# Optimization experiments

Measured on AMD Instinct MI355X. Metric: run time of the kernel, lower is better.

## Reference

```python
import jax, jax.numpy as jnp
import numpy as np

N, F, H, E = 100000, 128, 128, 3200000
EPS = 1e-5


def setup_inputs() -> dict:
    key = jax.random.key(0)
    ks = jax.random.split(key, 16)
    g = lambda k, shape, fan_in: jax.random.normal(k, shape, jnp.float32) / np.sqrt(fan_in)
    inp = {
        'x': jax.random.normal(ks[0], (N, F), jnp.float32),
        'edge_index': jax.random.randint(ks[1], (2, E), 0, N, jnp.int64),
        # SAGEConv params: lin_l (aggregated-neighbor path, has bias), lin_r (root path, no bias)
        'W1l': g(ks[2], (F, H), F), 'b1': jnp.zeros((H,), jnp.float32), 'W1r': g(ks[3], (F, H), F),
        'W2l': g(ks[4], (H, H), H), 'b2': jnp.zeros((H,), jnp.float32), 'W2r': g(ks[5], (H, H), H),
        'W3l': g(ks[6], (H, H), H), 'b3': jnp.zeros((H,), jnp.float32), 'W3r': g(ks[7], (H, H), H),
        'W4l': g(ks[8], (H, 1), H), 'b4': jnp.zeros((1,), jnp.float32), 'W4r': g(ks[9], (H, 1), H),
        # BatchNorm affine params
        'g1': jnp.ones((H,), jnp.float32), 'be1': jnp.zeros((H,), jnp.float32),
        'g2': jnp.ones((H,), jnp.float32), 'be2': jnp.zeros((H,), jnp.float32),
        'g3': jnp.ones((H,), jnp.float32), 'be3': jnp.zeros((H,), jnp.float32),
        # shared residual linear
        'Wlin': g(ks[10], (H, H), H), 'blin': jnp.zeros((H,), jnp.float32),
    }
    return inp


def _sage(x, src, dst, Wl, b, Wr):
    # mean aggregation of source features at destination nodes
    n = x.shape[0]
    s = jax.ops.segment_sum(x[src], dst, num_segments=n)          # [N, d]
    cnt = jax.ops.segment_sum(jnp.ones_like(dst, x.dtype), dst, num_segments=n)
    agg = s / jnp.maximum(cnt, 1.0)[:, None]
    return agg @ Wl + b + x @ Wr


def _bn(x, gamma, beta):
    # training-mode batch norm over node dim (biased variance, as torch)
    mu = x.mean(0)
    var = jnp.mean((x - mu) ** 2, axis=0)
    return gamma * (x - mu) * jax.lax.rsqrt(var + EPS) + beta


def reference(x, edge_index, W1l, b1, W1r, W2l, b2, W2r, W3l, b3, W3r,
              W4l, b4, W4r, g1, be1, g2, be2, g3, be3, Wlin, blin):
    src, dst = edge_index[0], edge_index[1]
    # dropout is identity (eval-mode reference)
    x1 = jax.nn.elu(_bn(_sage(x, src, dst, W1l, b1, W1r), g1, be1))
    x2 = jax.nn.elu(_bn(_sage(x1, src, dst, W2l, b2, W2r), g2, be2))
    x2 = x2 + x1 @ Wlin + blin
    x3 = jax.nn.elu(_bn(_sage(x2, src, dst, W3l, b3, W3r), g3, be3))
    x3 = x3 + x2 @ Wlin + blin
    x4 = _sage(x3, src, dst, W4l, b4, W4r)  # [N, 1]
    return jnp.squeeze(x4, -1)
```

## Files before the change

### kernel.cpp

```cpp
#include <hip/hip_runtime.h>
#include <hip/hip_bf16.h>
#include <math.h>

#define BN_EPS 1e-5f

typedef __attribute__((ext_vector_type(8))) short bf16x8;
typedef __attribute__((ext_vector_type(4))) float f32x4;
typedef unsigned int uint32;

__device__ __forceinline__ unsigned bf16rne(float f) {
  unsigned u = __float_as_uint(f);
  unsigned r = u + 0x7fffu + ((u >> 16) & 1u);
  return r >> 16;
}
__device__ __forceinline__ float bf2f_lo(uint32 u) { return __uint_as_float(u << 16); }
__device__ __forceinline__ float bf2f_hi(uint32 u) { return __uint_as_float(u & 0xffff0000u); }
__device__ __forceinline__ uint32 packbf2(float a, float b) {
  return bf16rne(a) | (bf16rne(b) << 16);
}

__device__ __forceinline__ int edge_at(const int* __restrict__ ei, long long idx, int is64) {
  return is64 ? ei[2 * idx] : ei[idx];
}

__global__ void detect_kernel(const int* __restrict__ ei, long long E, int* __restrict__ flag) {
  __shared__ int found;
  int t = threadIdx.x;
  if (t == 0) found = 0;
  __syncthreads();
  long long npairs = E < 1024 ? E : 1024;
  for (long long p = t; p < npairs; p += blockDim.x)
    if (ei[2 * p + 1] != 0) found = 1;
  __syncthreads();
  if (t == 0) *flag = found ? 0 : 1;
}

__global__ void zero_i32_kernel(int* __restrict__ p, long long n) {
  long long i = blockIdx.x * (long long)blockDim.x + threadIdx.x;
  if (i < n) p[i] = 0;
}
__global__ void zero_f32_kernel(float* __restrict__ p, long long n) {
  long long i = blockIdx.x * (long long)blockDim.x + threadIdx.x;
  if (i < n) p[i] = 0.f;
}

__global__ void extract_count_kernel(const int* __restrict__ ei, long long E,
                                     const int* __restrict__ flag,
                                     int* __restrict__ es, int* __restrict__ r8,
                                     int* __restrict__ cnt8, int N) {
  long long e = blockIdx.x * (long long)blockDim.x + threadIdx.x;
  if (e >= E) return;
  int is64 = *flag;
  es[e] = edge_at(ei, e, is64);
  int d = edge_at(ei, E + e, is64);
  int sh = blockIdx.x & 7;
  r8[e] = atomicAdd(&cnt8[(size_t)sh * N + d], 1);
}

__global__ void cumnode_kernel(const int* __restrict__ cnt8, int* __restrict__ cum8,
                               int* __restrict__ cnt_node, int N) {
  int n = blockIdx.x * blockDim.x + threadIdx.x;
  if (n >= N) return;
  int run = 0;
#pragma unroll
  for (int sh = 0; sh < 8; ++sh) {
    int c = cnt8[(size_t)sh * N + n];
    cum8[(size_t)sh * N + n] = run;
    run += c;
  }
  cnt_node[n] = run;
}

__global__ void partial_kernel(const int* __restrict__ cnt, int* __restrict__ bsum, int M) {
  __shared__ int s[256];
  int b = blockIdx.x, t = threadIdx.x;
  int base = b * 2048 + t * 8;
  int sum = 0;
#pragma unroll
  for (int i = 0; i < 8; ++i) {
    int idx = base + i;
    if (idx < M) sum += cnt[idx];
  }
  s[t] = sum;
  __syncthreads();
  for (int d = 128; d > 0; d >>= 1) {
    if (t < d) s[t] += s[t + d];
    __syncthreads();
  }
  if (t == 0) bsum[b] = s[0];
}

__global__ void scanb_kernel(int* __restrict__ bsum, int nb) {
  __shared__ int s[512];
  int t = threadIdx.x;
  int v = (t < nb) ? bsum[t] : 0;
  s[t] = v;
  __syncthreads();
  for (int d = 1; d < 512; d <<= 1) {
    int u = (t >= d) ? s[t - d] : 0;
    __syncthreads();
    s[t] += u;
    __syncthreads();
  }
  if (t < nb) bsum[t] = s[t] - v;
}

__global__ void offsets_kernel(const int* __restrict__ cnt, const int* __restrict__ bsum,
                               int* __restrict__ off, int M, long long Etot) {
  __shared__ int s[256];
  int b = blockIdx.x, t = threadIdx.x;
  int base = b * 2048 + t * 8;
  int v[8];
  int sum = 0;
#pragma unroll
  for (int i = 0; i < 8; ++i) {
    int idx = base + i;
    v[i] = (idx < M) ? cnt[idx] : 0;
    sum += v[i];
  }
  s[t] = sum;
  __syncthreads();
  for (int d = 1; d < 256; d <<= 1) {
    int u = (t >= d) ? s[t - d] : 0;
    __syncthreads();
    s[t] += u;
    __syncthreads();
  }
  int run = bsum[b] + s[t] - sum;
#pragma unroll
  for (int i = 0; i < 8; ++i) {
    int idx = base + i;
    if (idx < M) {
      off[idx] = run;
      run += v[i];
    }
  }
  if (b == 0 && t == 0) off[M] = (int)Etot;
}

__global__ void pos_kernel(const int* __restrict__ ei, long long E, const int* __restrict__ flag,
                           const int* __restrict__ r8, const int* __restrict__ off_node,
                           const int* __restrict__ cum8, uint32* __restrict__ ppk, int N) {
  long long e = blockIdx.x * (long long)blockDim.x + threadIdx.x;
  if (e >= E) return;
  int is64 = *flag;
  int d = edge_at(ei, E + e, is64);
  int sh = blockIdx.x & 7;
  uint32 pos = (uint32)(off_node[d] + cum8[(size_t)sh * N + d] + r8[e]);
  uint32 region = (uint32)d >> 15;
  ppk[e] = pos | (region << 28);
}

__global__ void scatter_det_kernel(const int* __restrict__ es, const uint32* __restrict__ ppk,
                                   long long E, uint32 p, int* __restrict__ esrc) {
  long long e = blockIdx.x * (long long)blockDim.x + threadIdx.x;
  if (e >= E) return;
  uint32 v = ppk[e];
  if ((v >> 28) == p) esrc[v & 0x0FFFFFFFu] = es[e];
}

__global__ void convert_bf16_kernel(const float* __restrict__ x, uint32* __restrict__ xb,
                                    long long total2) {
  long long i = blockIdx.x * (long long)blockDim.x + threadIdx.x;
  if (i >= total2) return;
  float2 f = ((const float2*)x)[i];
  xb[i] = packbf2(f.x, f.y);
}

__global__ void repack_all_kernel(const float* __restrict__ Wa, const float* __restrict__ Wb,
                                  const float* __restrict__ Wc, const float* __restrict__ Wd,
                                  const float* __restrict__ We, const float* __restrict__ Wf,
                                  const float* __restrict__ Wg, ushort* __restrict__ Wp) {
  int wi = blockIdx.x >> 3;
  const float* W = wi == 0 ? Wa : wi == 1 ? Wb : wi == 2 ? Wc : wi == 3 ? Wd
                 : wi == 4 ? We : wi == 5 ? Wf : Wg;
  ushort* dst = Wp + (size_t)wi * 16384;
  int s = (blockIdx.x & 7) * 256 + threadIdx.x;
  int nt = s >> 8, rem = s & 255, ks = rem >> 6, lane = rem & 63;
  int q = lane >> 4, l16 = lane & 15;
  int kbase = ks * 32 + q * 8, c = nt * 16 + l16;
  uint32 out[4];
#pragma unroll
  for (int jp = 0; jp < 4; ++jp) {
    float a = W[(size_t)(kbase + 2 * jp) * 128 + c];
    float b = W[(size_t)(kbase + 2 * jp + 1) * 128 + c];
    out[jp] = packbf2(a, b);
  }
  ((uint4*)dst)[s] = make_uint4(out[0], out[1], out[2], out[3]);
}

__global__ void aggregate_bf16_kernel(const uint32* __restrict__ X, const int* __restrict__ off,
                                      const int* __restrict__ esrc, uint32* __restrict__ out,
                                      int N) {
  int gw = (int)((blockIdx.x * (long long)blockDim.x + threadIdx.x) >> 6);
  int lane = threadIdx.x & 63;
  if (gw >= N) return;
  int b = off[gw], e = off[gw + 1];
  int sub = lane & 15, grp = lane >> 4;
  const uint4* X4 = (const uint4*)X;
  float acc[8];
#pragma unroll
  for (int j = 0; j < 8; ++j) acc[j] = 0.f;
  for (int i = b; i < e; i += 8) {
    int i0 = i + grp, i1 = i + 4 + grp;
    bool h0 = i0 < e, h1 = i1 < e;
    uint4 v0 = make_uint4(0, 0, 0, 0), v1 = make_uint4(0, 0, 0, 0);
    if (h0) { int s0 = esrc[i0]; v0 = X4[(size_t)s0 * 16 + sub]; }
    if (h1) { int s1 = esrc[i1]; v1 = X4[(size_t)s1 * 16 + sub]; }
    if (h0) {
      acc[0] += bf2f_lo(v0.x); acc[1] += bf2f_hi(v0.x);
      acc[2] += bf2f_lo(v0.y); acc[3] += bf2f_hi(v0.y);
      acc[4] += bf2f_lo(v0.z); acc[5] += bf2f_hi(v0.z);
      acc[6] += bf2f_lo(v0.w); acc[7] += bf2f_hi(v0.w);
    }
    if (h1) {
      acc[0] += bf2f_lo(v1.x); acc[1] += bf2f_hi(v1.x);
      acc[2] += bf2f_lo(v1.y); acc[3] += bf2f_hi(v1.y);
      acc[4] += bf2f_lo(v1.z); acc[5] += bf2f_hi(v1.z);
      acc[6] += bf2f_lo(v1.w); acc[7] += bf2f_hi(v1.w);
    }
  }
#pragma unroll
  for (int j = 0; j < 8; ++j) {
    acc[j] += __shfl_xor(acc[j], 16, 64);
    acc[j] += __shfl_xor(acc[j], 32, 64);
  }
  if (grp == 0) {
    float inv = 1.0f / fmaxf((float)(e - b), 1.0f);
    uint4 o;
    o.x = packbf2(acc[0] * inv, acc[1] * inv);
    o.y = packbf2(acc[2] * inv, acc[3] * inv);
    o.z = packbf2(acc[4] * inv, acc[5] * inv);
    o.w = packbf2(acc[6] * inv, acc[7] * inv);
    ((uint4*)out)[(size_t)gw * 16 + sub] = o;
  }
}

__launch_bounds__(256)
__global__ void gemm_mfma_kernel(const ushort* __restrict__ A1, const ushort* __restrict__ W1p,
                                 const ushort* __restrict__ A2, const ushort* __restrict__ W2p,
                                 const ushort* __restrict__ W3p,
                                 const float* __restrict__ bias, const float* __restrict__ rbias,
                                 ushort* __restrict__ Y, ushort* __restrict__ R,
                                 float* __restrict__ bnsum, int N) {
  __shared__ float sred[16][128];
  int t = threadIdx.x;
  int w = t >> 6, lane = t & 63;
  int quad = lane >> 4, l16 = lane & 15;
  int row0 = blockIdx.x * 64 + w * 16;

  f32x4 accY[8], accR[8];
#pragma unroll
  for (int nt = 0; nt < 8; ++nt) {
    accY[nt][0] = accY[nt][1] = accY[nt][2] = accY[nt][3] = 0.f;
    accR[nt][0] = accR[nt][1] = accR[nt][2] = accR[nt][3] = 0.f;
  }

  int rowA = row0 + l16;
  if (rowA > N - 1) rowA = N - 1;
  const ushort* a1p = A1 + (size_t)rowA * 128 + quad * 8;
  const ushort* a2p = A2 + (size_t)rowA * 128 + quad * 8;
  const int haveR = (W3p != nullptr);

#pragma unroll
  for (int ks = 0; ks < 4; ++ks) {
    bf16x8 a = *(const bf16x8*)(a1p + ks * 32);
#pragma unroll
    for (int nt = 0; nt < 8; ++nt) {
      bf16x8 b = *(const bf16x8*)(W1p + ((size_t)(nt * 4 + ks) * 64 + lane) * 8);
      accY[nt] = __builtin_amdgcn_mfma_f32_16x16x32_bf16(a, b, accY[nt], 0, 0, 0);
    }
  }
#pragma unroll
  for (int ks = 0; ks < 4; ++ks) {
    bf16x8 a = *(const bf16x8*)(a2p + ks * 32);
#pragma unroll
    for (int nt = 0; nt < 8; ++nt) {
      bf16x8 b = *(const bf16x8*)(W2p + ((size_t)(nt * 4 + ks) * 64 + lane) * 8);
      accY[nt] = __builtin_amdgcn_mfma_f32_16x16x32_bf16(a, b, accY[nt], 0, 0, 0);
    }
    if (haveR) {
#pragma unroll
      for (int nt = 0; nt < 8; ++nt) {
        bf16x8 b = *(const bf16x8*)(W3p + ((size_t)(nt * 4 + ks) * 64 + lane) * 8);
        accR[nt] = __builtin_amdgcn_mfma_f32_16x16x32_bf16(a, b, accR[nt], 0, 0, 0);
      }
    }
  }

  float s1v[8], s2v[8];
#pragma unroll
  for (int nt = 0; nt < 8; ++nt) {
    int c = nt * 16 + l16;
    float bv = bias[c];
    s1v[nt] = 0.f; s2v[nt] = 0.f;
#pragma unroll
    for (int reg = 0; reg < 4; ++reg) {
      int grow = row0 + quad * 4 + reg;
      if (grow < N) {
        float v = accY[nt][reg] + bv;
        Y[(size_t)grow * 128 + c] = (ushort)bf16rne(v);
        s1v[nt] += v; s2v[nt] += v * v;
      }
    }
    if (haveR) {
      float rb = rbias[c];
#pragma unroll
      for (int reg = 0; reg < 4; ++reg) {
        int grow = row0 + quad * 4 + reg;
        if (grow < N) {
          float v = accR[nt][reg] + rb;
          R[(size_t)grow * 128 + c] = (ushort)bf16rne(v);
        }
      }
    }
  }

  int rrow = w * 4 + quad;
#pragma unroll
  for (int nt = 0; nt < 8; ++nt) sred[rrow][nt * 16 + l16] = s1v[nt];
  __syncthreads();
  if (t < 128) {
    float tot = 0.f;
#pragma unroll
    for (int r16 = 0; r16 < 16; ++r16) tot += sred[r16][t];
    atomicAdd(&bnsum[(size_t)(blockIdx.x & 63) * 256 + t], tot);
  }
  __syncthreads();
#pragma unroll
  for (int nt = 0; nt < 8; ++nt) sred[rrow][nt * 16 + l16] = s2v[nt];
  __syncthreads();
  if (t < 128) {
    float tot = 0.f;
#pragma unroll
    for (int r16 = 0; r16 < 16; ++r16) tot += sred[r16][t];
    atomicAdd(&bnsum[(size_t)(blockIdx.x & 63) * 256 + 128 + t], tot);
  }
}

__global__ void bn_finalize_kernel(const float* __restrict__ bnsum, float* __restrict__ bnp, int N) {
  int t = threadIdx.x;
  if (t < 128) {
    float s = 0.f, s2 = 0.f;
    for (int sh = 0; sh < 64; ++sh) {
      s  += bnsum[(size_t)sh * 256 + t];
      s2 += bnsum[(size_t)sh * 256 + 128 + t];
    }
    float invN = 1.0f / (float)N;
    float mu = s * invN;
    float var = s2 * invN - mu * mu;
    bnp[t] = mu;
    bnp[128 + t] = rsqrtf(var + BN_EPS);
  }
}

__global__ void bn_elu_kernel(const uint32* __restrict__ Y, const float* __restrict__ bnp,
                              const float* __restrict__ g, const float* __restrict__ be,
                              const uint32* __restrict__ res, uint32* __restrict__ Xo,
                              long long total2) {
  long long i = blockIdx.x * (long long)blockDim.x + threadIdx.x;
  if (i >= total2) return;
  int c0 = (int)(i & 63) * 2;
  uint32 y = Y[i];
  float v0 = g[c0]     * (bf2f_lo(y) - bnp[c0])     * bnp[128 + c0]     + be[c0];
  float v1 = g[c0 + 1] * (bf2f_hi(y) - bnp[c0 + 1]) * bnp[128 + c0 + 1] + be[c0 + 1];
  v0 = v0 > 0.f ? v0 : expm1f(v0);
  v1 = v1 > 0.f ? v1 : expm1f(v1);
  if (res) {
    uint32 rv = res[i];
    v0 += bf2f_lo(rv); v1 += bf2f_hi(rv);
  }
  Xo[i] = packbf2(v0, v1);
}

__global__ void dot4_kernel(const uint32* __restrict__ X, const float* __restrict__ W4l,
                            const float* __restrict__ W4r, float* __restrict__ z,
                            float* __restrict__ rr, int N) {
  int gw = (int)((blockIdx.x * (long long)blockDim.x + threadIdx.x) >> 6);
  int lane = threadIdx.x & 63;
  if (gw >= N) return;
  uint32 u = X[(size_t)gw * 64 + lane];
  float x0 = bf2f_lo(u), x1 = bf2f_hi(u);
  float wl0 = W4l[2 * lane], wl1 = W4l[2 * lane + 1];
  float wr0 = W4r[2 * lane], wr1 = W4r[2 * lane + 1];
  float a = x0 * wl0 + x1 * wl1;
  float b = x0 * wr0 + x1 * wr1;
  for (int d = 32; d > 0; d >>= 1) {
    a += __shfl_down(a, d, 64);
    b += __shfl_down(b, d, 64);
  }
  if (lane == 0) { z[gw] = a; rr[gw] = b; }
}

__global__ void final_kernel(const float* __restrict__ z, const float* __restrict__ rr,
                             const int* __restrict__ off, const int* __restrict__ esrc,
                             const float* __restrict__ b4, float* __restrict__ out, int N) {
  int n = blockIdx.x * blockDim.x + threadIdx.x;
  if (n >= N) return;
  int b = off[n], e = off[n + 1];
  float s = 0.f;
  for (int i = b; i < e; ++i) s += z[esrc[i]];
  out[n] = s / fmaxf((float)(e - b), 1.0f) + b4[0] + rr[n];
}

extern "C" void kernel_launch(void* const* d_in, const int* in_sizes, int n_in,
                              void* d_out, int out_size, void* d_ws, size_t ws_size,
                              hipStream_t stream) {
  const float* x   = (const float*)d_in[0];
  const int*   ei  = (const int*)d_in[1];
  const float* W1l = (const float*)d_in[2];
  const float* b1  = (const float*)d_in[3];
  const float* W1r = (const float*)d_in[4];
  const float* W2l = (const float*)d_in[5];
  const float* b2  = (const float*)d_in[6];
  const float* W2r = (const float*)d_in[7];
  const float* W3l = (const float*)d_in[8];
  const float* b3  = (const float*)d_in[9];
  const float* W3r = (const float*)d_in[10];
  const float* W4l = (const float*)d_in[11];
  const float* b4  = (const float*)d_in[12];
  const float* W4r = (const float*)d_in[13];
  const float* g1  = (const float*)d_in[14];
  const float* be1 = (const float*)d_in[15];
  const float* g2  = (const float*)d_in[16];
  const float* be2 = (const float*)d_in[17];
  const float* g3  = (const float*)d_in[18];
  const float* be3 = (const float*)d_in[19];
  const float* Wlin= (const float*)d_in[20];
  const float* blin= (const float*)d_in[21];

  const int N = in_sizes[0] / 128;
  const long long E = in_sizes[1] / 2;
  const int M = 8 * N;
  float* out = (float*)d_out;

  char* w = (char*)d_ws;
  size_t o = 0;
  auto alloc = [&](size_t bytes) -> char* {
    char* p = w + o;
    o = (o + bytes + 255) & ~(size_t)255;
    return p;
  };
  int*    off_node = (int*)alloc((size_t)(N + 1) * 4);
  int*    cnt_node = (int*)alloc((size_t)N * 4);
  int*    bsum     = (int*)alloc(512 * 4);
  int*    flag     = (int*)alloc(4);
  float*  bnsum    = (float*)alloc((size_t)64 * 256 * 4);
  float*  bnp      = (float*)alloc(256 * 4);
  float*  z        = (float*)alloc((size_t)N * 4);
  float*  rr       = (float*)alloc((size_t)N * 4);
  ushort* Wp       = (ushort*)alloc((size_t)7 * 2048 * 16);
  int*    esrc     = (int*)alloc((size_t)E * 4);
  size_t slotA = (size_t)2 * E * 4;
  size_t ysz = (size_t)N * 256;
  if (ysz > slotA) slotA = ysz;
  char* poolA  = alloc(slotA);
  char* poolB1 = alloc((size_t)N * 256);
  char* poolB3 = alloc((size_t)N * 256);
  uint32* B2   = (uint32*)alloc((size_t)N * 256);
  (void)ws_size; (void)n_in; (void)out_size;

  int*    es    = (int*)poolA;
  int*    r8    = (int*)(poolA + (size_t)E * 4);
  ushort* Ybuf  = (ushort*)poolA;
  int*    cnt8  = (int*)poolB1;
  int*    cum8  = cnt8 + M;
  uint32* ppk   = (uint32*)(cum8 + M);
  uint32* B1    = (uint32*)poolB1;
  uint32* B3    = (uint32*)poolB3;

  const int B = 256;
  const int eb  = (int)((E + B - 1) / B);
  const int nb  = (N + B - 1) / B;
  const int wb  = (int)(((long long)N * 64 + B - 1) / B);
  const int gb  = (N + 63) / 64;
  const long long tot2 = (long long)N * 64;
  const int cb  = (int)((tot2 + B - 1) / B);
  const int gN  = (N + 2047) / 2048;

  ushort* Wp1l = Wp + 0 * 16384;
  ushort* Wp1r = Wp + 1 * 16384;
  ushort* Wp2l = Wp + 2 * 16384;
  ushort* Wp2r = Wp + 3 * 16384;
  ushort* Wp3l = Wp + 4 * 16384;
  ushort* Wp3r = Wp + 5 * 16384;
  ushort* Wpln = Wp + 6 * 16384;

  detect_kernel<<<1, 1024, 0, stream>>>(ei, E, flag);
  zero_i32_kernel<<<(M + B - 1) / B, B, 0, stream>>>(cnt8, (long long)M);
  extract_count_kernel<<<eb, B, 0, stream>>>(ei, E, flag, es, r8, cnt8, N);
  cumnode_kernel<<<nb, B, 0, stream>>>(cnt8, cum8, cnt_node, N);
  partial_kernel<<<gN, B, 0, stream>>>(cnt_node, bsum, N);
  scanb_kernel<<<1, 512, 0, stream>>>(bsum, gN);
  offsets_kernel<<<gN, B, 0, stream>>>(cnt_node, bsum, off_node, N, E);
  pos_kernel<<<eb, B, 0, stream>>>(ei, E, flag, r8, off_node, cum8, ppk, N);
  for (uint32 p = 0; p < 4; ++p)
    scatter_det_kernel<<<eb, B, 0, stream>>>(es, ppk, E, p, esrc);

  convert_bf16_kernel<<<cb, B, 0, stream>>>(x, B1, tot2);
  repack_all_kernel<<<56, B, 0, stream>>>(W1l, W1r, W2l, W2r, W3l, W3r, Wlin, Wp);

  aggregate_bf16_kernel<<<wb, B, 0, stream>>>(B1, off_node, esrc, B2, N);
  zero_f32_kernel<<<64, B, 0, stream>>>(bnsum, 64 * 256);
  gemm_mfma_kernel<<<gb, B, 0, stream>>>((const ushort*)B2, Wp1l, (const ushort*)B1, Wp1r,
                                         nullptr, b1, nullptr, Ybuf, nullptr, bnsum, N);
  bn_finalize_kernel<<<1, 128, 0, stream>>>(bnsum, bnp, N);
  bn_elu_kernel<<<cb, B, 0, stream>>>((const uint32*)Ybuf, bnp, g1, be1, nullptr, B3, tot2);

  aggregate_bf16_kernel<<<wb, B, 0, stream>>>(B3, off_node, esrc, B2, N);
  zero_f32_kernel<<<64, B, 0, stream>>>(bnsum, 64 * 256);
  gemm_mfma_kernel<<<gb, B, 0, stream>>>((const ushort*)B2, Wp2l, (const ushort*)B3, Wp2r,
                                         Wpln, b2, blin, Ybuf, (ushort*)B1, bnsum, N);
  bn_finalize_kernel<<<1, 128, 0, stream>>>(bnsum, bnp, N);
  bn_elu_kernel<<<cb, B, 0, stream>>>((const uint32*)Ybuf, bnp, g2, be2, B1, B2, tot2);

  aggregate_bf16_kernel<<<wb, B, 0, stream>>>(B2, off_node, esrc, B3, N);
  zero_f32_kernel<<<64, B, 0, stream>>>(bnsum, 64 * 256);
  gemm_mfma_kernel<<<gb, B, 0, stream>>>((const ushort*)B3, Wp3l, (const ushort*)B2, Wp3r,
                                         Wpln, b3, blin, Ybuf, (ushort*)B1, bnsum, N);
  bn_finalize_kernel<<<1, 128, 0, stream>>>(bnsum, bnp, N);
  bn_elu_kernel<<<cb, B, 0, stream>>>((const uint32*)Ybuf, bnp, g3, be3, B1, B3, tot2);

  dot4_kernel<<<wb, B, 0, stream>>>(B3, W4l, W4r, z, rr, N);
  final_kernel<<<nb, B, 0, stream>>>(z, rr, off_node, esrc, b4, out, N);
}
```

Measured before the change: 997.8 us.

## Fuse CSR build, input conversion and tail kernels; single-shard counting

Merges flag detection and buffer zeroing into one init kernel. Edge counting (now a single counter array instead of 8 shards), feature bf16 conversion and weight repacking go into one multi-role build kernel. Position computation is fused with the first scatter pass, and edge sources are read straight from edge_index instead of a staged copy. The aggregation loop is unrolled to issue 4 gathers per step, BN-sum zeroing moves into bn_finalize, and the final dot products are fused into the last bn_elu. The goal is fewer launches and less intermediate traffic, at the risk of more atomic contention on the unsharded counters.

```diff
diff --git a/kernel.cpp b/kernel.cpp
--- a/kernel.cpp
+++ b/kernel.cpp
@@ -23,52 +23,90 @@
   return is64 ? ei[2 * idx] : ei[idx];
 }
 
-__global__ void detect_kernel(const int* __restrict__ ei, long long E, int* __restrict__ flag) {
-  __shared__ int found;
-  int t = threadIdx.x;
-  if (t == 0) found = 0;
-  __syncthreads();
-  long long npairs = E < 1024 ? E : 1024;
-  for (long long p = t; p < npairs; p += blockDim.x)
-    if (ei[2 * p + 1] != 0) found = 1;
-  __syncthreads();
-  if (t == 0) *flag = found ? 0 : 1;
-}
-
-__global__ void zero_i32_kernel(int* __restrict__ p, long long n) {
-  long long i = blockIdx.x * (long long)blockDim.x + threadIdx.x;
-  if (i < n) p[i] = 0;
-}
-__global__ void zero_f32_kernel(float* __restrict__ p, long long n) {
-  long long i = blockIdx.x * (long long)blockDim.x + threadIdx.x;
-  if (i < n) p[i] = 0.f;
-}
-
-__global__ void extract_count_kernel(const int* __restrict__ ei, long long E,
-                                     const int* __restrict__ flag,
-                                     int* __restrict__ es, int* __restrict__ r8,
-                                     int* __restrict__ cnt8, int N) {
-  long long e = blockIdx.x * (long long)blockDim.x + threadIdx.x;
-  if (e >= E) return;
-  int is64 = *flag;
-  es[e] = edge_at(ei, e, is64);
-  int d = edge_at(ei, E + e, is64);
-  int sh = blockIdx.x & 7;
-  r8[e] = atomicAdd(&cnt8[(size_t)sh * N + d], 1);
-}
-
-__global__ void cumnode_kernel(const int* __restrict__ cnt8, int* __restrict__ cum8,
-                               int* __restrict__ cnt_node, int N) {
-  int n = blockIdx.x * blockDim.x + threadIdx.x;
-  if (n >= N) return;
-  int run = 0;
-#pragma unroll
-  for (int sh = 0; sh < 8; ++sh) {
-    int c = cnt8[(size_t)sh * N + n];
-    cum8[(size_t)sh * N + n] = run;
-    run += c;
-  }
-  cnt_node[n] = run;
+__global__ void init_kernel(const int* __restrict__ ei, long long E, int* __restrict__ flag,
+                            int* __restrict__ cnt, float* __restrict__ bnsum, int N) {
+  if (blockIdx.x == 0) {
+    __shared__ int found;
+    int t = threadIdx.x;
+    if (t == 0) found = 0;
+    __syncthreads();
+    long long npairs = E < 1024 ? E : 1024;
+    for (long long p = t; p < npairs; p += blockDim.x)
+      if (ei[2 * p + 1] != 0) found = 1;
+    __syncthreads();
+    if (t == 0) *flag = found ? 0 : 1;
+    return;
+  }
+  long long i = (blockIdx.x - 1) * (long long)blockDim.x + threadIdx.x;
+  if (i < N) cnt[i] = 0;
+  else if (i < (long long)N + 64 * 256) bnsum[i - N] = 0.f;
+}
+
+__launch_bounds__(256)
+__global__ void build_kernel(const int* __restrict__ ei, long long E,
+                             const int* __restrict__ flag,
+                             int* __restrict__ r, int* __restrict__ cnt,
+                             const float* __restrict__ x, uint32* __restrict__ xb,
+                             long long nf4,
+                             const float* __restrict__ Wa, const float* __restrict__ Wb,
+                             const float* __restrict__ Wc, const float* __restrict__ Wd,
+                             const float* __restrict__ We, const float* __restrict__ Wf,
+                             const float* __restrict__ Wg, ushort* __restrict__ Wp,
+                             long long K3) {
+  long long b = blockIdx.x;
+  if (b >= K3) {
+    int rb = (int)(b - K3);
+    int wi = rb >> 3;
+    const float* W = wi == 0 ? Wa : wi == 1 ? Wb : wi == 2 ? Wc : wi == 3 ? Wd
+                   : wi == 4 ? We : wi == 5 ? Wf : Wg;
+    ushort* dst = Wp + (size_t)wi * 16384;
+    int s = (rb & 7) * 256 + threadIdx.x;
+    int nt = s >> 8, rem = s & 255, ks = rem >> 6, lane = rem & 63;
+    int q = lane >> 4, l16 = lane & 15;
+    int kbase = ks * 32 + q * 8, c = nt * 16 + l16;
+    uint32 o[4];
+#pragma unroll
+    for (int jp = 0; jp < 4; ++jp) {
+      float fa = W[(size_t)(kbase + 2 * jp) * 128 + c];
+      float fb = W[(size_t)(kbase + 2 * jp + 1) * 128 + c];
+      o[jp] = packbf2(fa, fb);
+    }
+    ((uint4*)dst)[s] = make_uint4(o[0], o[1], o[2], o[3]);
+    return;
+  }
+  int role = (int)(b % 3);
+  long long id = b / 3;
+  if (role == 0) {
+    long long g = id * 256 + threadIdx.x;
+    long long e0 = 2 * g;
+    if (e0 >= E) return;
+    int is64 = *flag;
+    bool h1 = (e0 + 1 < E);
+    int d0, d1 = 0;
+    if (is64 && !(E & 1)) {
+      int4 dv = ((const int4*)(ei + 2 * E))[g];
+      d0 = dv.x; d1 = dv.z;
+    } else {
+      d0 = edge_at(ei, E + e0, is64);
+      if (h1) d1 = edge_at(ei, E + e0 + 1, is64);
+    }
+    int r0 = atomicAdd(&cnt[d0], 1);
+    if (h1) {
+      int r1 = atomicAdd(&cnt[d1], 1);
+      ((int2*)r)[g] = make_int2(r0, r1);
+    } else {
+      r[e0] = r0;
+    }
+  } else {
+    long long i = (id * 2 + (role - 1)) * 256 + threadIdx.x;
+    if (i < nf4) {
+      float4 f = ((const float4*)x)[i];
+      uint2 o;
+      o.x = packbf2(f.x, f.y);
+      o.y = packbf2(f.z, f.w);
+      ((uint2*)xb)[i] = o;
+    }
+  }
 }
 
 __global__ void partial_kernel(const int* __restrict__ cnt, int* __restrict__ bsum, int M) {
@@ -138,55 +176,46 @@
   if (b == 0 && t == 0) off[M] = (int)Etot;
 }
 
-__global__ void pos_kernel(const int* __restrict__ ei, long long E, const int* __restrict__ flag,
-                           const int* __restrict__ r8, const int* __restrict__ off_node,
-                           const int* __restrict__ cum8, uint32* __restrict__ ppk, int N) {
-  long long e = blockIdx.x * (long long)blockDim.x + threadIdx.x;
-  if (e >= E) return;
+__global__ void pos_scatter_kernel(const int* __restrict__ ei, long long E,
+                                   const int* __restrict__ flag, const int* __restrict__ r,
+                                   const int* __restrict__ off, uint32* __restrict__ ppk,
+                                   int* __restrict__ esrc) {
+  long long g = blockIdx.x * (long long)blockDim.x + threadIdx.x;
+  long long e0 = 2 * g;
+  if (e0 >= E) return;
   int is64 = *flag;
-  int d = edge_at(ei, E + e, is64);
-  int sh = blockIdx.x & 7;
-  uint32 pos = (uint32)(off_node[d] + cum8[(size_t)sh * N + d] + r8[e]);
-  uint32 region = (uint32)d >> 15;
-  ppk[e] = pos | (region << 28);
-}
-
-__global__ void scatter_det_kernel(const int* __restrict__ es, const uint32* __restrict__ ppk,
-                                   long long E, uint32 p, int* __restrict__ esrc) {
+  bool h1 = (e0 + 1 < E);
+  int d0, d1 = 0;
+  if (is64 && !(E & 1)) {
+    int4 dv = ((const int4*)(ei + 2 * E))[g];
+    d0 = dv.x; d1 = dv.z;
+  } else {
+    d0 = edge_at(ei, E + e0, is64);
+    if (h1) d1 = edge_at(ei, E + e0 + 1, is64);
+  }
+  int r0, r1 = 0;
+  if (h1) { int2 rv = ((const int2*)r)[g]; r0 = rv.x; r1 = rv.y; }
+  else r0 = r[e0];
+  uint32 p0 = (uint32)(off[d0] + r0);
+  uint32 reg0 = (uint32)d0 >> 15;
+  ppk[e0] = p0 | (reg0 << 28);
+  if (reg0 == 0) esrc[p0] = edge_at(ei, e0, is64);
+  if (h1) {
+    uint32 p1 = (uint32)(off[d1] + r1);
+    uint32 reg1 = (uint32)d1 >> 15;
+    ppk[e0 + 1] = p1 | (reg1 << 28);
+    if (reg1 == 0) esrc[p1] = edge_at(ei, e0 + 1, is64);
+  }
+}
+
+__global__ void scatter_det_kernel(const int* __restrict__ ei, long long E,
+                                   const int* __restrict__ flag,
+                                   const uint32* __restrict__ ppk, uint32 p,
+                                   int* __restrict__ esrc) {
   long long e = blockIdx.x * (long long)blockDim.x + threadIdx.x;
   if (e >= E) return;
   uint32 v = ppk[e];
-  if ((v >> 28) == p) esrc[v & 0x0FFFFFFFu] = es[e];
-}
-
-__global__ void convert_bf16_kernel(const float* __restrict__ x, uint32* __restrict__ xb,
-                                    long long total2) {
-  long long i = blockIdx.x * (long long)blockDim.x + threadIdx.x;
-  if (i >= total2) return;
-  float2 f = ((const float2*)x)[i];
-  xb[i] = packbf2(f.x, f.y);
-}
-
-__global__ void repack_all_kernel(const float* __restrict__ Wa, const float* __restrict__ Wb,
-                                  const float* __restrict__ Wc, const float* __restrict__ Wd,
-                                  const float* __restrict__ We, const float* __restrict__ Wf,
-                                  const float* __restrict__ Wg, ushort* __restrict__ Wp) {
-  int wi = blockIdx.x >> 3;
-  const float* W = wi == 0 ? Wa : wi == 1 ? Wb : wi == 2 ? Wc : wi == 3 ? Wd
-                 : wi == 4 ? We : wi == 5 ? Wf : Wg;
-  ushort* dst = Wp + (size_t)wi * 16384;
-  int s = (blockIdx.x & 7) * 256 + threadIdx.x;
-  int nt = s >> 8, rem = s & 255, ks = rem >> 6, lane = rem & 63;
-  int q = lane >> 4, l16 = lane & 15;
-  int kbase = ks * 32 + q * 8, c = nt * 16 + l16;
-  uint32 out[4];
-#pragma unroll
-  for (int jp = 0; jp < 4; ++jp) {
-    float a = W[(size_t)(kbase + 2 * jp) * 128 + c];
-    float b = W[(size_t)(kbase + 2 * jp + 1) * 128 + c];
-    out[jp] = packbf2(a, b);
-  }
-  ((uint4*)dst)[s] = make_uint4(out[0], out[1], out[2], out[3]);
+  if ((v >> 28) == p) esrc[v & 0x0FFFFFFFu] = edge_at(ei, e, *flag);
 }
 
 __global__ void aggregate_bf16_kernel(const uint32* __restrict__ X, const int* __restrict__ off,
@@ -201,23 +230,20 @@
   float acc[8];
 #pragma unroll
   for (int j = 0; j < 8; ++j) acc[j] = 0.f;
-  for (int i = b; i < e; i += 8) {
-    int i0 = i + grp, i1 = i + 4 + grp;
-    bool h0 = i0 < e, h1 = i1 < e;
-    uint4 v0 = make_uint4(0, 0, 0, 0), v1 = make_uint4(0, 0, 0, 0);
-    if (h0) { int s0 = esrc[i0]; v0 = X4[(size_t)s0 * 16 + sub]; }
-    if (h1) { int s1 = esrc[i1]; v1 = X4[(size_t)s1 * 16 + sub]; }
-    if (h0) {
-      acc[0] += bf2f_lo(v0.x); acc[1] += bf2f_hi(v0.x);
-      acc[2] += bf2f_lo(v0.y); acc[3] += bf2f_hi(v0.y);
-      acc[4] += bf2f_lo(v0.z); acc[5] += bf2f_hi(v0.z);
-      acc[6] += bf2f_lo(v0.w); acc[7] += bf2f_hi(v0.w);
-    }
-    if (h1) {
-      acc[0] += bf2f_lo(v1.x); acc[1] += bf2f_hi(v1.x);
-      acc[2] += bf2f_lo(v1.y); acc[3] += bf2f_hi(v1.y);
-      acc[4] += bf2f_lo(v1.z); acc[5] += bf2f_hi(v1.z);
-      acc[6] += bf2f_lo(v1.w); acc[7] += bf2f_hi(v1.w);
+  for (int i = b; i < e; i += 16) {
+    uint4 v[4];
+#pragma unroll
+    for (int u = 0; u < 4; ++u) {
+      int ii = i + u * 4 + grp;
+      v[u] = make_uint4(0, 0, 0, 0);
+      if (ii < e) { int s = esrc[ii]; v[u] = X4[(size_t)s * 16 + sub]; }
+    }
+#pragma unroll
+    for (int u = 0; u < 4; ++u) {
+      acc[0] += bf2f_lo(v[u].x); acc[1] += bf2f_hi(v[u].x);
+      acc[2] += bf2f_lo(v[u].y); acc[3] += bf2f_hi(v[u].y);
+      acc[4] += bf2f_lo(v[u].z); acc[5] += bf2f_hi(v[u].z);
+      acc[6] += bf2f_lo(v[u].w); acc[7] += bf2f_hi(v[u].w);
     }
   }
 #pragma unroll
@@ -338,7 +364,7 @@
   }
 }
 
-__global__ void bn_finalize_kernel(const float* __restrict__ bnsum, float* __restrict__ bnp, int N) {
+__global__ void bn_finalize_kernel(float* __restrict__ bnsum, float* __restrict__ bnp, int N) {
   int t = threadIdx.x;
   if (t < 128) {
     float s = 0.f, s2 = 0.f;
@@ -352,11 +378,15 @@
     bnp[t] = mu;
     bnp[128 + t] = rsqrtf(var + BN_EPS);
   }
+  __syncthreads();
+  for (int i = t; i < 64 * 256; i += 256) bnsum[i] = 0.f;
 }
 
 __global__ void bn_elu_kernel(const uint32* __restrict__ Y, const float* __restrict__ bnp,
                               const float* __restrict__ g, const float* __restrict__ be,
                               const uint32* __restrict__ res, uint32* __restrict__ Xo,
+                              const float* __restrict__ W4l, const float* __restrict__ W4r,
+                              float* __restrict__ z, float* __restrict__ rr,
                               long long total2) {
   long long i = blockIdx.x * (long long)blockDim.x + threadIdx.x;
   if (i >= total2) return;
@@ -370,26 +400,20 @@
     uint32 rv = res[i];
     v0 += bf2f_lo(rv); v1 += bf2f_hi(rv);
   }
-  Xo[i] = packbf2(v0, v1);
-}
-
-__global__ void dot4_kernel(const uint32* __restrict__ X, const float* __restrict__ W4l,
-                            const float* __restrict__ W4r, float* __restrict__ z,
-                            float* __restrict__ rr, int N) {
-  int gw = (int)((blockIdx.x * (long long)blockDim.x + threadIdx.x) >> 6);
-  int lane = threadIdx.x & 63;
-  if (gw >= N) return;
-  uint32 u = X[(size_t)gw * 64 + lane];
-  float x0 = bf2f_lo(u), x1 = bf2f_hi(u);
-  float wl0 = W4l[2 * lane], wl1 = W4l[2 * lane + 1];
-  float wr0 = W4r[2 * lane], wr1 = W4r[2 * lane + 1];
-  float a = x0 * wl0 + x1 * wl1;
-  float b = x0 * wr0 + x1 * wr1;
-  for (int d = 32; d > 0; d >>= 1) {
-    a += __shfl_down(a, d, 64);
-    b += __shfl_down(b, d, 64);
-  }
-  if (lane == 0) { z[gw] = a; rr[gw] = b; }
+  if (Xo) Xo[i] = packbf2(v0, v1);
+  if (z) {
+    float a = v0 * W4l[c0] + v1 * W4l[c0 + 1];
+    float bb = v0 * W4r[c0] + v1 * W4r[c0 + 1];
+    for (int d = 32; d > 0; d >>= 1) {
+      a += __shfl_down(a, d, 64);
+      bb += __shfl_down(bb, d, 64);
+    }
+    if ((i & 63) == 0) {
+      long long row = i >> 6;
+      z[row] = a;
+      rr[row] = bb;
+    }
+  }
 }
 
 __global__ void final_kernel(const float* __restrict__ z, const float* __restrict__ rr,
@@ -431,7 +455,6 @@
 
   const int N = in_sizes[0] / 128;
   const long long E = in_sizes[1] / 2;
-  const int M = 8 * N;
   float* out = (float*)d_out;
 
   char* w = (char*)d_ws;
@@ -442,7 +465,6 @@
     return p;
   };
   int*    off_node = (int*)alloc((size_t)(N + 1) * 4);
-  int*    cnt_node = (int*)alloc((size_t)N * 4);
   int*    bsum     = (int*)alloc(512 * 4);
   int*    flag     = (int*)alloc(4);
   float*  bnsum    = (float*)alloc((size_t)64 * 256 * 4);
@@ -451,32 +473,41 @@
   float*  rr       = (float*)alloc((size_t)N * 4);
   ushort* Wp       = (ushort*)alloc((size_t)7 * 2048 * 16);
   int*    esrc     = (int*)alloc((size_t)E * 4);
-  size_t slotA = (size_t)2 * E * 4;
+  size_t slotA = (size_t)E * 4;
   size_t ysz = (size_t)N * 256;
   if (ysz > slotA) slotA = ysz;
-  char* poolA  = alloc(slotA);
-  char* poolB1 = alloc((size_t)N * 256);
-  char* poolB3 = alloc((size_t)N * 256);
-  uint32* B2   = (uint32*)alloc((size_t)N * 256);
+  char* poolA = alloc(slotA);
+  char* B1c   = alloc((size_t)N * 256);
+  char* B2c   = alloc((size_t)N * 256);
+  char* B3c   = alloc((size_t)N * 256);
   (void)ws_size; (void)n_in; (void)out_size;
 
-  int*    es    = (int*)poolA;
-  int*    r8    = (int*)(poolA + (size_t)E * 4);
-  ushort* Ybuf  = (ushort*)poolA;
-  int*    cnt8  = (int*)poolB1;
-  int*    cum8  = cnt8 + M;
-  uint32* ppk   = (uint32*)(cum8 + M);
-  uint32* B1    = (uint32*)poolB1;
-  uint32* B3    = (uint32*)poolB3;
+  int*    r    = (int*)poolA;
+  ushort* Ybuf = (ushort*)poolA;
+  uint32* B1   = (uint32*)B1c;
+  uint32* B2   = (uint32*)B2c;
+  uint32* B3   = (uint32*)B3c;
+  size_t cnt_bytes = ((size_t)N * 4 + 255) & ~(size_t)255;
+  size_t csr_need = cnt_bytes + (size_t)E * 4;
+  char* poolCSR = (csr_need <= (size_t)N * 256) ? B3c : alloc(csr_need);
+  int*    cnt = (int*)poolCSR;
+  uint32* ppk = (uint32*)(poolCSR + cnt_bytes);
 
   const int B = 256;
-  const int eb  = (int)((E + B - 1) / B);
-  const int nb  = (N + B - 1) / B;
-  const int wb  = (int)(((long long)N * 64 + B - 1) / B);
-  const int gb  = (N + 63) / 64;
+  const long long pairs = (E + 1) / 2;
+  const int ebp = (int)((pairs + B - 1) / B);
+  const long long nf4 = (long long)N * 32;
+  const int cb4 = (int)((nf4 + B - 1) / B);
+  int K = ebp > (cb4 + 1) / 2 ? ebp : (cb4 + 1) / 2;
+  const int Gbuild = 3 * K + 56;
+  const int eb = (int)((E + B - 1) / B);
+  const int zb = 1 + (int)(((long long)N + 64 * 256 + B - 1) / B);
+  const int nb = (N + B - 1) / B;
+  const int wb = (int)(((long long)N * 64 + B - 1) / B);
+  const int gb = (N + 63) / 64;
   const long long tot2 = (long long)N * 64;
-  const int cb  = (int)((tot2 + B - 1) / B);
-  const int gN  = (N + 2047) / 2048;
+  const int cb = (int)((tot2 + B - 1) / B);
+  const int gN = (N + 2047) / 2048;
 
   ushort* Wp1l = Wp + 0 * 16384;
   ushort* Wp1r = Wp + 1 * 16384;
@@ -486,41 +517,37 @@
   ushort* Wp3r = Wp + 5 * 16384;
   ushort* Wpln = Wp + 6 * 16384;
 
-  detect_kernel<<<1, 1024, 0, stream>>>(ei, E, flag);
-  zero_i32_kernel<<<(M + B - 1) / B, B, 0, stream>>>(cnt8, (long long)M);
-  extract_count_kernel<<<eb, B, 0, stream>>>(ei, E, flag, es, r8, cnt8, N);
-  cumnode_kernel<<<nb, B, 0, stream>>>(cnt8, cum8, cnt_node, N);
-  partial_kernel<<<gN, B, 0, stream>>>(cnt_node, bsum, N);
+  init_kernel<<<zb, B, 0, stream>>>(ei, E, flag, cnt, bnsum, N);
+  build_kernel<<<Gbuild, B, 0, stream>>>(ei, E, flag, r, cnt, x, B2, nf4,
+                                         W1l, W1r, W2l, W2r, W3l, W3r, Wlin, Wp,
+                                         (long long)3 * K);
+  partial_kernel<<<gN, B, 0, stream>>>(cnt, bsum, N);
   scanb_kernel<<<1, 512, 0, stream>>>(bsum, gN);
-  offsets_kernel<<<gN, B, 0, stream>>>(cnt_node, bsum, off_node, N, E);
-  pos_kernel<<<eb, B, 0, stream>>>(ei, E, flag, r8, off_node, cum8, ppk, N);
-  for (uint32 p = 0; p < 4; ++p)
-    scatter_det_kernel<<<eb, B, 0, stream>>>(es, ppk, E, p, esrc);
-
-  convert_bf16_kernel<<<cb, B, 0, stream>>>(x, B1, tot2);
-  repack_all_kernel<<<56, B, 0, stream>>>(W1l, W1r, W2l, W2r, W3l, W3r, Wlin, Wp);
-
-  aggregate_bf16_kernel<<<wb, B, 0, stream>>>(B1, off_node, esrc, B2, N);
-  zero_f32_kernel<<<64, B, 0, stream>>>(bnsum, 64 * 256);
-  gemm_mfma_kernel<<<gb, B, 0, stream>>>((const ushort*)B2, Wp1l, (const ushort*)B1, Wp1r,
+  offsets_kernel<<<gN, B, 0, stream>>>(cnt, bsum, off_node, N, E);
+  pos_scatter_kernel<<<ebp, B, 0, stream>>>(ei, E, flag, r, off_node, ppk, esrc);
+  for (uint32 p = 1; p < 4; ++p)
+    scatter_det_kernel<<<eb, B, 0, stream>>>(ei, E, flag, ppk, p, esrc);
+
+  aggregate_bf16_kernel<<<wb, B, 0, stream>>>(B2, off_node, esrc, B1, N);
+  gemm_mfma_kernel<<<gb, B, 0, stream>>>((const ushort*)B1, Wp1l, (const ushort*)B2, Wp1r,
                                          nullptr, b1, nullptr, Ybuf, nullptr, bnsum, N);
-  bn_finalize_kernel<<<1, 128, 0, stream>>>(bnsum, bnp, N);
-  bn_elu_kernel<<<cb, B, 0, stream>>>((const uint32*)Ybuf, bnp, g1, be1, nullptr, B3, tot2);
-
-  aggregate_bf16_kernel<<<wb, B, 0, stream>>>(B3, off_node, esrc, B2, N);
-  zero_f32_kernel<<<64, B, 0, stream>>>(bnsum, 64 * 256);
-  gemm_mfma_kernel<<<gb, B, 0, stream>>>((const ushort*)B2, Wp2l, (const ushort*)B3, Wp2r,
-                                         Wpln, b2, blin, Ybuf, (ushort*)B1, bnsum, N);
-  bn_finalize_kernel<<<1, 128, 0, stream>>>(bnsum, bnp, N);
-  bn_elu_kernel<<<cb, B, 0, stream>>>((const uint32*)Ybuf, bnp, g2, be2, B1, B2, tot2);
-
-  aggregate_bf16_kernel<<<wb, B, 0, stream>>>(B2, off_node, esrc, B3, N);
-  zero_f32_kernel<<<64, B, 0, stream>>>(bnsum, 64 * 256);
-  gemm_mfma_kernel<<<gb, B, 0, stream>>>((const ushort*)B3, Wp3l, (const ushort*)B2, Wp3r,
-                                         Wpln, b3, blin, Ybuf, (ushort*)B1, bnsum, N);
-  bn_finalize_kernel<<<1, 128, 0, stream>>>(bnsum, bnp, N);
-  bn_elu_kernel<<<cb, B, 0, stream>>>((const uint32*)Ybuf, bnp, g3, be3, B1, B3, tot2);
-
-  dot4_kernel<<<wb, B, 0, stream>>>(B3, W4l, W4r, z, rr, N);
+  bn_finalize_kernel<<<1, 256, 0, stream>>>(bnsum, bnp, N);
+  bn_elu_kernel<<<cb, B, 0, stream>>>((const uint32*)Ybuf, bnp, g1, be1, nullptr, B3,
+                                      nullptr, nullptr, nullptr, nullptr, tot2);
+
+  aggregate_bf16_kernel<<<wb, B, 0, stream>>>(B3, off_node, esrc, B1, N);
+  gemm_mfma_kernel<<<gb, B, 0, stream>>>((const ushort*)B1, Wp2l, (const ushort*)B3, Wp2r,
+                                         Wpln, b2, blin, Ybuf, (ushort*)B2, bnsum, N);
+  bn_finalize_kernel<<<1, 256, 0, stream>>>(bnsum, bnp, N);
+  bn_elu_kernel<<<cb, B, 0, stream>>>((const uint32*)Ybuf, bnp, g2, be2, B2, B1,
+                                      nullptr, nullptr, nullptr, nullptr, tot2);
+
+  aggregate_bf16_kernel<<<wb, B, 0, stream>>>(B1, off_node, esrc, B3, N);
+  gemm_mfma_kernel<<<gb, B, 0, stream>>>((const ushort*)B3, Wp3l, (const ushort*)B1, Wp3r,
+                                         Wpln, b3, blin, Ybuf, (ushort*)B2, bnsum, N);
+  bn_finalize_kernel<<<1, 256, 0, stream>>>(bnsum, bnp, N);
+  bn_elu_kernel<<<cb, B, 0, stream>>>((const uint32*)Ybuf, bnp, g3, be3, B2, nullptr,
+                                      W4l, W4r, z, rr, tot2);
+
   final_kernel<<<nb, B, 0, stream>>>(z, rr, off_node, esrc, b4, out, N);
 }
```

Result: faster. 968.1 us (-3.0%).
